# Kernel optimization log

Measured on AMD Instinct MI355X. Metric: run time of the kernel, lower is better.

The kernel has to match this reference:

```python
import jax, jax.numpy as jnp
import numpy as np

N = 50000
E = 800000
IN_DIM = 256
HID = 256
OUT_DIM = 2


def setup_inputs() -> dict:
    key = jax.random.key(0)
    ks = jax.random.split(key, 10)
    x = jax.random.normal(ks[0], (N, IN_DIM), dtype=jnp.float32)
    edge_index = jax.random.randint(ks[1], (2, E), 0, N, dtype=jnp.int64)
    # Glorot-ish scaling so activations stay well-conditioned through 4 layers
    def w(k, fan_in, fan_out):
        return jax.random.normal(k, (fan_in, fan_out), dtype=jnp.float32) / jnp.sqrt(jnp.float32(fan_in))
    return {
        "x": x,
        "edge_index": edge_index,
        "W0": w(ks[2], IN_DIM, HID), "b0": jnp.zeros((HID,), jnp.float32),
        "W1": w(ks[3], HID, HID),    "b1": jnp.zeros((HID,), jnp.float32),
        "W2": w(ks[4], HID, HID),    "b2": jnp.zeros((HID,), jnp.float32),
        "W3": w(ks[5], HID, OUT_DIM), "b3": jnp.zeros((OUT_DIM,), jnp.float32),
    }


def _gcn_norm(edge_index, n, dtype):
    # PyG gcn_norm with self-loops: deg over destination, norm = d^-1/2[src]*d^-1/2[dst]
    loops = jnp.arange(n, dtype=edge_index.dtype)
    src = jnp.concatenate([edge_index[0], loops])
    dst = jnp.concatenate([edge_index[1], loops])
    deg = jax.ops.segment_sum(jnp.ones_like(dst, dtype=dtype), dst, num_segments=n)
    dis = deg ** -0.5  # deg >= 1 due to self-loops
    norm = dis[src] * dis[dst]
    return src, dst, norm


def reference(x, edge_index, W0, b0, W1, b1, W2, b2, W3, b3):
    n = x.shape[0]
    src, dst, norm = _gcn_norm(edge_index, n, x.dtype)

    def conv(h, W, b):
        h = h @ W                              # [N, F_out] dense GEMM
        msg = h[src] * norm[:, None]           # edge-gather + scale
        agg = jax.ops.segment_sum(msg, dst, num_segments=n)  # scatter-add
        return agg + b

    h = jax.nn.relu(conv(x, W0, b0))
    h = jax.nn.relu(conv(h, W1, b1))
    h = jax.nn.relu(conv(h, W2, b2))
    return conv(h, W3, b3)
```

## Files before the change

kernel.cpp:

```cpp
#include <hip/hip_runtime.h>

#define N_NODES 50000
#define N_EDGES 800000

static inline int cdiv(int a, int b) { return (a + b - 1) / b; }

typedef __attribute__((ext_vector_type(8))) short bf16x8;
typedef __attribute__((ext_vector_type(4))) float f32x4;
typedef __attribute__((ext_vector_type(2))) float f32x2;
typedef __attribute__((ext_vector_type(4))) unsigned int u32x4;

static __device__ __forceinline__ unsigned short f2bf(float f) {
    unsigned int u = __float_as_uint(f);
    unsigned int r = (u + 0x7FFF + ((u >> 16) & 1)) >> 16;
    return (unsigned short)r;
}
static __device__ __forceinline__ float bf2f(unsigned short h) {
    return __uint_as_float((unsigned int)h << 16);
}
static __device__ __forceinline__ float bf_lo(unsigned int u) { return __uint_as_float(u << 16); }
static __device__ __forceinline__ float bf_hi(unsigned int u) { return __uint_as_float(u & 0xFFFF0000u); }

static __device__ __forceinline__ int2 ldnt2(const int2* p) {
    unsigned long long u = __builtin_nontemporal_load((const unsigned long long*)p);
    int2 r;
    r.x = (int)(u & 0xFFFFFFFFull);
    r.y = (int)(u >> 32);
    return r;
}

static __device__ __forceinline__ void acc8p(f32x2* acc, uint4 v, float wgt) {
    f32x2 w2;
    w2.x = wgt;
    w2.y = wgt;
    f32x2 p;
    p.x = bf_lo(v.x); p.y = bf_hi(v.x); acc[0] += p * w2;
    p.x = bf_lo(v.y); p.y = bf_hi(v.y); acc[1] += p * w2;
    p.x = bf_lo(v.z); p.y = bf_hi(v.z); acc[2] += p * w2;
    p.x = bf_lo(v.w); p.y = bf_hi(v.w); acc[3] += p * w2;
}


__global__ void k_count(const int* __restrict__ edst, int* cnt, int e) {
    int i = (blockIdx.x * 256 + threadIdx.x) * 4;
    if (i + 3 < e) {
        int4 v = *(const int4*)(edst + i);
        atomicAdd(&cnt[v.x], 1);
        atomicAdd(&cnt[v.y], 1);
        atomicAdd(&cnt[v.z], 1);
        atomicAdd(&cnt[v.w], 1);
    } else {
        for (int k = i; k < e; ++k) atomicAdd(&cnt[edst[k]], 1);
    }
}

__global__ __launch_bounds__(256) void k_scan1(const int* __restrict__ cnt,
                                               int* __restrict__ row_ptr,
                                               float* __restrict__ dis,
                                               int* __restrict__ blk, int n) {
    __shared__ int sums[256];
    int t = threadIdx.x;
    int base = blockIdx.x * 1024 + t * 4;
    int c0 = 0, c1 = 0, c2 = 0, c3 = 0;
    if (base + 3 < n) {
        int4 v = *(const int4*)(cnt + base);
        c0 = v.x + 1; c1 = v.y + 1; c2 = v.z + 1; c3 = v.w + 1;
    } else {
        if (base + 0 < n) c0 = cnt[base + 0] + 1;
        if (base + 1 < n) c1 = cnt[base + 1] + 1;
        if (base + 2 < n) c2 = cnt[base + 2] + 1;
        if (base + 3 < n) c3 = cnt[base + 3] + 1;
    }
    int s = c0 + c1 + c2 + c3;
    sums[t] = s;
    __syncthreads();
    int x = s;
    for (int off = 1; off < 256; off <<= 1) {
        int y = (t >= off) ? sums[t - off] : 0;
        __syncthreads();
        x += y;
        sums[t] = x;
        __syncthreads();
    }
    int excl = x - s;
    if (base + 0 < n) { row_ptr[base + 0] = excl;                dis[base + 0] = rsqrtf((float)c0); }
    if (base + 1 < n) { row_ptr[base + 1] = excl + c0;           dis[base + 1] = rsqrtf((float)c1); }
    if (base + 2 < n) { row_ptr[base + 2] = excl + c0 + c1;      dis[base + 2] = rsqrtf((float)c2); }
    if (base + 3 < n) { row_ptr[base + 3] = excl + c0 + c1 + c2; dis[base + 3] = rsqrtf((float)c3); }
    if (t == 255) blk[blockIdx.x] = x;
}

__global__ __launch_bounds__(256) void k_scan2(int* __restrict__ blk,
                                               int* __restrict__ row_ptr_n, int nb) {
    __shared__ int sums[256];
    int t = threadIdx.x;
    int s = (t < nb) ? blk[t] : 0;
    sums[t] = s;
    __syncthreads();
    int x = s;
    for (int off = 1; off < 256; off <<= 1) {
        int y = (t >= off) ? sums[t - off] : 0;
        __syncthreads();
        x += y;
        sums[t] = x;
        __syncthreads();
    }
    if (t < nb) blk[t] = x - s;
    if (t == 255) row_ptr_n[0] = x;
}

__global__ __launch_bounds__(256) void k_scan3(int* __restrict__ row_ptr,
                                               int* __restrict__ pos,
                                               const int* __restrict__ blk, int n) {
    int base = blockIdx.x * 1024 + threadIdx.x * 4;
    int off = blk[blockIdx.x];
#pragma unroll
    for (int i = 0; i < 4; ++i) {
        int idx = base + i;
        if (idx < n) {
            int v = row_ptr[idx] + off;
            row_ptr[idx] = v;
            pos[idx] = v;
        }
    }
}

__global__ void k_fill(const int* __restrict__ esrc, const int* __restrict__ edst,
                       int* pos, const float* __restrict__ dis,
                       int2* __restrict__ eg, int e, int n) {
    int i = blockIdx.x * 256 + threadIdx.x;
    if (i < e) {
        int s = esrc[i], d = edst[i];
        int p = atomicAdd(&pos[d], 1);
        unsigned long long u = (unsigned long long)(unsigned int)s |
                               ((unsigned long long)(unsigned int)__float_as_int(dis[s] * dis[d]) << 32);
        __builtin_nontemporal_store(u, (unsigned long long*)&eg[p]);
    } else if (i < e + n) {
        int v = i - e;
        int p = atomicAdd(&pos[v], 1);
        float dv = dis[v];
        unsigned long long u = (unsigned long long)(unsigned int)v |
                               ((unsigned long long)(unsigned int)__float_as_int(dv * dv) << 32);
        __builtin_nontemporal_store(u, (unsigned long long*)&eg[p]);
    }
}


__global__ __launch_bounds__(256) void k_prep(const float* __restrict__ W0,
                                              const float* __restrict__ W1,
                                              const float* __restrict__ W2,
                                              const float* __restrict__ b0,
                                              const float* __restrict__ b1,
                                              const float* __restrict__ b2,
                                              const float* __restrict__ W3,
                                              unsigned short* __restrict__ Wth,
                                              unsigned short* __restrict__ Wtl,
                                              float* __restrict__ bpw,
                                              const float* __restrict__ X,
                                              unsigned short* __restrict__ Xh, long total4) {
    if (blockIdx.x < 48) {
        __shared__ float tile[64][65];
        int layer = blockIdx.x / 16;
        int tid = blockIdx.x % 16;
        int ti = tid >> 2, tj = tid & 3;
        const float* W = layer == 0 ? W0 : (layer == 1 ? W1 : W2);
        int r0 = ti * 64, n0 = tj * 64;
        int rr = threadIdx.x >> 4;
        int cc = (threadIdx.x & 15) * 4;
#pragma unroll
        for (int j = 0; j < 4; ++j) {
            float4 v = *(const float4*)(W + (size_t)(r0 + rr + j * 16) * 256 + n0 + cc);
            tile[rr + j * 16][cc + 0] = v.x;
            tile[rr + j * 16][cc + 1] = v.y;
            tile[rr + j * 16][cc + 2] = v.z;
            tile[rr + j * 16][cc + 3] = v.w;
        }
        __syncthreads();
        int pl = threadIdx.x & 63;
        int ng = threadIdx.x >> 6;
        int kl = (layer != 0) ? ((pl & 3) * 16 + (pl >> 2)) : pl;
#pragma unroll
        for (int i = 0; i < 16; ++i) {
            int nl = ng * 16 + i;
            float v = tile[kl][nl];
            unsigned short h = f2bf(v);
            size_t o = (size_t)layer * 65536 + (size_t)(n0 + nl) * 256 + r0 + pl;
            Wth[o] = h;
            Wtl[o] = f2bf(v - bf2f(h));
        }
    } else if (blockIdx.x == 48) {
        int p = threadIdx.x;
        int pl = p & 63;
        int c = (p & ~63) + (pl & 3) * 16 + (pl >> 2);
        bpw[p] = b0[c];
        bpw[256 + p] = b1[c];
        bpw[512 + p] = b2[c];
        bpw[768 + p * 2 + 0] = W3[(size_t)c * 2 + 0];
        bpw[768 + p * 2 + 1] = W3[(size_t)c * 2 + 1];
    } else {
        long i = (long)(blockIdx.x - 49) * 256 + threadIdx.x;
        if (i >= total4) return;
        float4 v = *(const float4*)(X + i * 4);
        ushort4 h;
        h.x = f2bf(v.x);
        h.y = f2bf(v.y);
        h.z = f2bf(v.z);
        h.w = f2bf(v.w);
        *(ushort4*)(Xh + i * 4) = h;
    }
}


#define GEMM_RB 196

__global__ __launch_bounds__(256) void k_gemm_mfma(const unsigned short* __restrict__ Ah,
                                                   const unsigned short* __restrict__ Wth,
                                                   const unsigned short* __restrict__ Wtl,
                                                   unsigned short* __restrict__ C, int M) {
    __shared__ unsigned short Wh[64][264];
    __shared__ unsigned short Wl[64][136];
    int rowblk = blockIdx.x % GEMM_RB;
    int colblk = blockIdx.x / GEMM_RB;
    int c0 = colblk * 64;
    int m0 = rowblk * 256;
    int t = threadIdx.x;
    int sr = t >> 2;

    {
        int hk0 = (t & 3) * 64;
        const unsigned short* gh = Wth + (size_t)(c0 + sr) * 256 + hk0;
        unsigned short* lh = &Wh[sr][hk0];
#pragma unroll
        for (int i = 0; i < 8; ++i)
            *(uint4*)(lh + i * 8) = *(const uint4*)(gh + i * 8);
        int lk0 = (t & 3) * 32;
        const unsigned short* gl = Wtl + (size_t)(c0 + sr) * 256 + lk0;
        unsigned short* ll = &Wl[sr][lk0];
#pragma unroll
        for (int i = 0; i < 4; ++i)
            *(uint4*)(ll + i * 8) = *(const uint4*)(gl + i * 8);
    }
    __syncthreads();

    int lane = t & 63, wave = t >> 6;
    int quad = lane >> 4, l16 = lane & 15;

    const unsigned short* aph[4];
#pragma unroll
    for (int mt = 0; mt < 4; ++mt) {
        int m = m0 + wave * 64 + mt * 16 + l16;
        if (m >= M) m = M - 1;
        aph[mt] = Ah + (size_t)m * 256 + quad * 8;
    }

    f32x4 acc[4][4];
#pragma unroll
    for (int i = 0; i < 4; ++i)
#pragma unroll
        for (int j = 0; j < 4; ++j) acc[i][j] = (f32x4){0.f, 0.f, 0.f, 0.f};

#pragma unroll 2
    for (int kc = 0; kc < 4; ++kc) {
        int ko = kc * 32;
        bf16x8 ahf[4];
#pragma unroll
        for (int mt = 0; mt < 4; ++mt) ahf[mt] = *(const bf16x8*)(aph[mt] + ko);
#pragma unroll
        for (int nt = 0; nt < 4; ++nt) {
            bf16x8 bh = *(const bf16x8*)&Wh[nt * 16 + l16][ko + quad * 8];
            bf16x8 bl = *(const bf16x8*)&Wl[nt * 16 + l16][ko + quad * 8];
#pragma unroll
            for (int mt = 0; mt < 4; ++mt) {
                acc[mt][nt] = __builtin_amdgcn_mfma_f32_16x16x32_bf16(ahf[mt], bh, acc[mt][nt], 0, 0, 0);
                acc[mt][nt] = __builtin_amdgcn_mfma_f32_16x16x32_bf16(ahf[mt], bl, acc[mt][nt], 0, 0, 0);
            }
        }
    }

    __syncthreads();
    {
        int lk0 = (t & 3) * 32;
        const unsigned short* gl = Wtl + (size_t)(c0 + sr) * 256 + 128 + lk0;
        unsigned short* ll = &Wl[sr][lk0];
#pragma unroll
        for (int i = 0; i < 4; ++i)
            *(uint4*)(ll + i * 8) = *(const uint4*)(gl + i * 8);
    }
    __syncthreads();

#pragma unroll 2
    for (int kc = 4; kc < 8; ++kc) {
        int ko = kc * 32;
        int kol = ko - 128;
        bf16x8 ahf[4];
#pragma unroll
        for (int mt = 0; mt < 4; ++mt) ahf[mt] = *(const bf16x8*)(aph[mt] + ko);
#pragma unroll
        for (int nt = 0; nt < 4; ++nt) {
            bf16x8 bh = *(const bf16x8*)&Wh[nt * 16 + l16][ko + quad * 8];
            bf16x8 bl = *(const bf16x8*)&Wl[nt * 16 + l16][kol + quad * 8];
#pragma unroll
            for (int mt = 0; mt < 4; ++mt) {
                acc[mt][nt] = __builtin_amdgcn_mfma_f32_16x16x32_bf16(ahf[mt], bh, acc[mt][nt], 0, 0, 0);
                acc[mt][nt] = __builtin_amdgcn_mfma_f32_16x16x32_bf16(ahf[mt], bl, acc[mt][nt], 0, 0, 0);
            }
        }
    }

#pragma unroll
    for (int mt = 0; mt < 4; ++mt) {
#pragma unroll
        for (int r = 0; r < 4; ++r) {
            int row = m0 + wave * 64 + mt * 16 + quad * 4 + r;
            if (row < M) {
                ushort4 sv;
                sv.x = f2bf(acc[mt][0][r]);
                sv.y = f2bf(acc[mt][1][r]);
                sv.z = f2bf(acc[mt][2][r]);
                sv.w = f2bf(acc[mt][3][r]);
                *(ushort4*)(C + (size_t)row * 256 + c0 + l16 * 4) = sv;
            }
        }
    }
}


template <int MODE>
__global__ __launch_bounds__(256, 8) void k_agg256(const unsigned short* __restrict__ t,
                                                   const int* __restrict__ row_ptr,
                                                   const int2* __restrict__ eg,
                                                   const float* __restrict__ bp,
                                                   unsigned short* __restrict__ outh,
                                                   const float* __restrict__ w3p,
                                                   float* __restrict__ t2, int n) {
    int lane = threadIdx.x & 63;
    int wave = threadIdx.x >> 6;
    int node = blockIdx.x * 4 + wave;
    if (node >= n) return;
    int half = lane >> 5;
    int fl = lane & 31;
    int beg = row_ptr[node], end = row_ptr[node + 1];
    f32x2 acc2[4];
#pragma unroll
    for (int i = 0; i < 4; ++i) { acc2[i].x = 0.f; acc2[i].y = 0.f; }
    const unsigned short* tp = t + fl * 8;

    int e = beg + half;
    for (; e + 10 < end; e += 12) {
        int2 a0 = ldnt2(eg + e), a1 = ldnt2(eg + e + 2), a2 = ldnt2(eg + e + 4);
        int2 a3 = ldnt2(eg + e + 6), a4 = ldnt2(eg + e + 8), a5 = ldnt2(eg + e + 10);
        uint4 v0 = *(const uint4*)(tp + (size_t)a0.x * 256);
        uint4 v1 = *(const uint4*)(tp + (size_t)a1.x * 256);
        uint4 v2 = *(const uint4*)(tp + (size_t)a2.x * 256);
        uint4 v3 = *(const uint4*)(tp + (size_t)a3.x * 256);
        uint4 v4 = *(const uint4*)(tp + (size_t)a4.x * 256);
        uint4 v5 = *(const uint4*)(tp + (size_t)a5.x * 256);
        acc8p(acc2, v0, __int_as_float(a0.y));
        acc8p(acc2, v1, __int_as_float(a1.y));
        acc8p(acc2, v2, __int_as_float(a2.y));
        acc8p(acc2, v3, __int_as_float(a3.y));
        acc8p(acc2, v4, __int_as_float(a4.y));
        acc8p(acc2, v5, __int_as_float(a5.y));
    }
    for (; e + 6 < end; e += 8) {
        int2 a0 = ldnt2(eg + e), a1 = ldnt2(eg + e + 2);
        int2 a2 = ldnt2(eg + e + 4), a3 = ldnt2(eg + e + 6);
        uint4 v0 = *(const uint4*)(tp + (size_t)a0.x * 256);
        uint4 v1 = *(const uint4*)(tp + (size_t)a1.x * 256);
        uint4 v2 = *(const uint4*)(tp + (size_t)a2.x * 256);
        uint4 v3 = *(const uint4*)(tp + (size_t)a3.x * 256);
        acc8p(acc2, v0, __int_as_float(a0.y));
        acc8p(acc2, v1, __int_as_float(a1.y));
        acc8p(acc2, v2, __int_as_float(a2.y));
        acc8p(acc2, v3, __int_as_float(a3.y));
    }
    for (; e + 2 < end; e += 4) {
        int2 a0 = ldnt2(eg + e), a1 = ldnt2(eg + e + 2);
        uint4 v0 = *(const uint4*)(tp + (size_t)a0.x * 256);
        uint4 v1 = *(const uint4*)(tp + (size_t)a1.x * 256);
        acc8p(acc2, v0, __int_as_float(a0.y));
        acc8p(acc2, v1, __int_as_float(a1.y));
    }
    if (e < end) {
        int2 a0 = ldnt2(eg + e);
        uint4 v0 = *(const uint4*)(tp + (size_t)a0.x * 256);
        acc8p(acc2, v0, __int_as_float(a0.y));
    }

    float va[8];
#pragma unroll
    for (int i = 0; i < 4; ++i) { va[2 * i] = acc2[i].x; va[2 * i + 1] = acc2[i].y; }
#pragma unroll
    for (int i = 0; i < 8; ++i) va[i] += __shfl_xor(va[i], 32);

    if (MODE == 0) {
        if (half == 0) {
            float4 bA = *(const float4*)(bp + fl * 8);
            float4 bB = *(const float4*)(bp + fl * 8 + 4);
            float r0 = fmaxf(va[0] + bA.x, 0.f), r1 = fmaxf(va[1] + bA.y, 0.f);
            float r2 = fmaxf(va[2] + bA.z, 0.f), r3 = fmaxf(va[3] + bA.w, 0.f);
            float r4 = fmaxf(va[4] + bB.x, 0.f), r5 = fmaxf(va[5] + bB.y, 0.f);
            float r6 = fmaxf(va[6] + bB.z, 0.f), r7 = fmaxf(va[7] + bB.w, 0.f);
            u32x4 w;
            w.x = (unsigned)f2bf(r0) | ((unsigned)f2bf(r1) << 16);
            w.y = (unsigned)f2bf(r2) | ((unsigned)f2bf(r3) << 16);
            w.z = (unsigned)f2bf(r4) | ((unsigned)f2bf(r5) << 16);
            w.w = (unsigned)f2bf(r6) | ((unsigned)f2bf(r7) << 16);
            __builtin_nontemporal_store(w, (u32x4*)(outh + (size_t)node * 256 + fl * 8));
        }
    } else {
        float4 bA = *(const float4*)(bp + fl * 8);
        float4 bB = *(const float4*)(bp + fl * 8 + 4);
        float r0 = fmaxf(va[0] + bA.x, 0.f), r1 = fmaxf(va[1] + bA.y, 0.f);
        float r2 = fmaxf(va[2] + bA.z, 0.f), r3 = fmaxf(va[3] + bA.w, 0.f);
        float r4 = fmaxf(va[4] + bB.x, 0.f), r5 = fmaxf(va[5] + bB.y, 0.f);
        float r6 = fmaxf(va[6] + bB.z, 0.f), r7 = fmaxf(va[7] + bB.w, 0.f);
        const float* wp = w3p + fl * 16;
        float4 wA = *(const float4*)(wp + 0);
        float4 wB = *(const float4*)(wp + 4);
        float4 wC = *(const float4*)(wp + 8);
        float4 wD = *(const float4*)(wp + 12);
        float s0 = r0 * wA.x + r1 * wA.z + r2 * wB.x + r3 * wB.z +
                   r4 * wC.x + r5 * wC.z + r6 * wD.x + r7 * wD.z;
        float s1 = r0 * wA.y + r1 * wA.w + r2 * wB.y + r3 * wB.w +
                   r4 * wC.y + r5 * wC.w + r6 * wD.y + r7 * wD.w;
#pragma unroll
        for (int off = 16; off > 0; off >>= 1) {
            s0 += __shfl_xor(s0, off);
            s1 += __shfl_xor(s1, off);
        }
        if (lane == 0) {
            f32x2 o;
            o.x = s0;
            o.y = s1;
            __builtin_nontemporal_store(o, (f32x2*)(t2 + (size_t)node * 2));
        }
    }
}


__global__ void k_agg2(const float* __restrict__ t2,
                       const int* __restrict__ row_ptr,
                       const int2* __restrict__ eg,
                       const float* __restrict__ b3,
                       float* __restrict__ out, int n) {
    int tid = blockIdx.x * 256 + threadIdx.x;
    int node = tid >> 2;
    int sub = tid & 3;
    if (node >= n) return;
    int beg = row_ptr[node], end = row_ptr[node + 1];
    float a0 = 0.f, a1 = 0.f;
    for (int e = beg + sub; e < end; e += 4) {
        int2 m = ldnt2(eg + e);
        float w = __int_as_float(m.y);
        float2 v = *(const float2*)(t2 + (size_t)m.x * 2);
        a0 += w * v.x;
        a1 += w * v.y;
    }
    a0 += __shfl_xor(a0, 1); a1 += __shfl_xor(a1, 1);
    a0 += __shfl_xor(a0, 2); a1 += __shfl_xor(a1, 2);
    if (sub == 0) {
        out[(size_t)node * 2 + 0] = a0 + b3[0];
        out[(size_t)node * 2 + 1] = a1 + b3[1];
    }
}


extern "C" void kernel_launch(void* const* d_in, const int* in_sizes, int n_in,
                              void* d_out, int out_size, void* d_ws, size_t ws_size,
                              hipStream_t stream) {
    const int N = N_NODES, E = N_EDGES;
    const float* x  = (const float*)d_in[0];
    const int* ei   = (const int*)d_in[1];
    const int* esrc = ei;
    const int* edst = ei + E;
    const float* W0 = (const float*)d_in[2];
    const float* b0 = (const float*)d_in[3];
    const float* W1 = (const float*)d_in[4];
    const float* b1 = (const float*)d_in[5];
    const float* W2 = (const float*)d_in[6];
    const float* b2 = (const float*)d_in[7];
    const float* W3 = (const float*)d_in[8];
    const float* b3 = (const float*)d_in[9];
    float* out = (float*)d_out;

    unsigned short* Ahh = (unsigned short*)d_ws;
    unsigned short* Tb  = Ahh + (size_t)N * 256;
    unsigned short* Wth = Tb + (size_t)N * 256;
    unsigned short* Wtl = Wth + 3 * 65536;
    int2*  eg     = (int2*)(Wtl + 3 * 65536);
    float* t2     = (float*)(eg + (E + N));
    float* bpw    = t2 + (size_t)N * 2;
    float* dis    = bpw + 1280;
    int*   cnt    = (int*)(dis + N);
    int*   row_ptr= cnt + N;
    int*   pos    = row_ptr + (N + 1);
    int*   blk    = pos + N;

    const int NB = cdiv(N, 1024);

    hipMemsetAsync(cnt, 0, (size_t)N * sizeof(int), stream);
    k_count<<<cdiv(E, 1024), 256, 0, stream>>>(edst, cnt, E);
    k_scan1<<<NB, 256, 0, stream>>>(cnt, row_ptr, dis, blk, N);
    k_scan2<<<1, 256, 0, stream>>>(blk, row_ptr + N, NB);
    k_scan3<<<NB, 256, 0, stream>>>(row_ptr, pos, blk, N);
    k_fill<<<cdiv(E + N, 256), 256, 0, stream>>>(esrc, edst, pos, dis, eg, E, N);

    const int ggrid = GEMM_RB * 4;
    const int agrid = cdiv(N, 4);
    const long total4 = (long)N * 64;
    const int CA = cdiv((int)total4, 256);

    k_prep<<<49 + CA, 256, 0, stream>>>(W0, W1, W2, b0, b1, b2, W3, Wth, Wtl, bpw, x, Ahh, total4);

    k_gemm_mfma<<<ggrid, 256, 0, stream>>>(Ahh, Wth, Wtl, Tb, N);
    k_agg256<0><<<agrid, 256, 0, stream>>>(Tb, row_ptr, eg, bpw, Ahh, nullptr, nullptr, N);
    k_gemm_mfma<<<ggrid, 256, 0, stream>>>(Ahh, Wth + 65536, Wtl + 65536, Tb, N);
    k_agg256<0><<<agrid, 256, 0, stream>>>(Tb, row_ptr, eg, bpw + 256, Ahh, nullptr, nullptr, N);
    k_gemm_mfma<<<ggrid, 256, 0, stream>>>(Ahh, Wth + 2 * 65536, Wtl + 2 * 65536, Tb, N);
    k_agg256<1><<<agrid, 256, 0, stream>>>(Tb, row_ptr, eg, bpw + 512, nullptr, bpw + 768, t2, N);
    k_agg2<<<cdiv(4 * N, 256), 256, 0, stream>>>(t2, row_ptr, eg, b3, out, N);
}
```

Measured before the change: 466.3 us.

## Fuse degree count into prep kernel and remap GEMM blocks for XCD locality

Merges the edge-degree counting kernel with the weight/input bf16 prep kernel into a single launch, removing one kernel launch and letting the two independent workloads overlap. It also remaps GEMM block indices so the four column blocks sharing a row block run on the same XCD (blockIdx & 7), improving L2 reuse of the A rows. The GEMM grid is rounded up to a multiple of 8 row blocks, which adds a few blocks that exit early.

```diff
diff --git a/kernel.cpp b/kernel.cpp
--- a/kernel.cpp
+++ b/kernel.cpp
@@ -41,18 +41,85 @@
 }
 
 
-__global__ void k_count(const int* __restrict__ edst, int* cnt, int e) {
-    int i = (blockIdx.x * 256 + threadIdx.x) * 4;
-    if (i + 3 < e) {
-        int4 v = *(const int4*)(edst + i);
-        atomicAdd(&cnt[v.x], 1);
-        atomicAdd(&cnt[v.y], 1);
-        atomicAdd(&cnt[v.z], 1);
-        atomicAdd(&cnt[v.w], 1);
+#define CNT_B (((N_EDGES) + 1023) / 1024)
+
+__global__ __launch_bounds__(256) void k_init(const int* __restrict__ edst, int* cnt, int e,
+                                              const float* __restrict__ W0,
+                                              const float* __restrict__ W1,
+                                              const float* __restrict__ W2,
+                                              const float* __restrict__ b0,
+                                              const float* __restrict__ b1,
+                                              const float* __restrict__ b2,
+                                              const float* __restrict__ W3,
+                                              unsigned short* __restrict__ Wth,
+                                              unsigned short* __restrict__ Wtl,
+                                              float* __restrict__ bpw,
+                                              const float* __restrict__ X,
+                                              unsigned short* __restrict__ Xh, long total4) {
+    if (blockIdx.x < CNT_B) {
+        int i = (blockIdx.x * 256 + threadIdx.x) * 4;
+        if (i + 3 < e) {
+            int4 v = *(const int4*)(edst + i);
+            atomicAdd(&cnt[v.x], 1);
+            atomicAdd(&cnt[v.y], 1);
+            atomicAdd(&cnt[v.z], 1);
+            atomicAdd(&cnt[v.w], 1);
+        } else {
+            for (int k = i; k < e; ++k) atomicAdd(&cnt[edst[k]], 1);
+        }
+    } else if (blockIdx.x < CNT_B + 48) {
+        __shared__ float tile[64][65];
+        int wb = blockIdx.x - CNT_B;
+        int layer = wb / 16;
+        int tid = wb % 16;
+        int ti = tid >> 2, tj = tid & 3;
+        const float* W = layer == 0 ? W0 : (layer == 1 ? W1 : W2);
+        int r0 = ti * 64, n0 = tj * 64;
+        int rr = threadIdx.x >> 4;
+        int cc = (threadIdx.x & 15) * 4;
+#pragma unroll
+        for (int j = 0; j < 4; ++j) {
+            float4 v = *(const float4*)(W + (size_t)(r0 + rr + j * 16) * 256 + n0 + cc);
+            tile[rr + j * 16][cc + 0] = v.x;
+            tile[rr + j * 16][cc + 1] = v.y;
+            tile[rr + j * 16][cc + 2] = v.z;
+            tile[rr + j * 16][cc + 3] = v.w;
+        }
+        __syncthreads();
+        int pl = threadIdx.x & 63;
+        int ng = threadIdx.x >> 6;
+        int kl = (layer != 0) ? ((pl & 3) * 16 + (pl >> 2)) : pl;
+#pragma unroll
+        for (int i = 0; i < 16; ++i) {
+            int nl = ng * 16 + i;
+            float v = tile[kl][nl];
+            unsigned short h = f2bf(v);
+            size_t o = (size_t)layer * 65536 + (size_t)(n0 + nl) * 256 + r0 + pl;
+            Wth[o] = h;
+            Wtl[o] = f2bf(v - bf2f(h));
+        }
+    } else if (blockIdx.x == CNT_B + 48) {
+        int p = threadIdx.x;
+        int pl = p & 63;
+        int c = (p & ~63) + (pl & 3) * 16 + (pl >> 2);
+        bpw[p] = b0[c];
+        bpw[256 + p] = b1[c];
+        bpw[512 + p] = b2[c];
+        bpw[768 + p * 2 + 0] = W3[(size_t)c * 2 + 0];
+        bpw[768 + p * 2 + 1] = W3[(size_t)c * 2 + 1];
     } else {
-        for (int k = i; k < e; ++k) atomicAdd(&cnt[edst[k]], 1);
-    }
-}
+        long i = (long)(blockIdx.x - (CNT_B + 49)) * 256 + threadIdx.x;
+        if (i >= total4) return;
+        float4 v = *(const float4*)(X + i * 4);
+        ushort4 h;
+        h.x = f2bf(v.x);
+        h.y = f2bf(v.y);
+        h.z = f2bf(v.z);
+        h.w = f2bf(v.w);
+        *(ushort4*)(Xh + i * 4) = h;
+    }
+}
+
 
 __global__ __launch_bounds__(256) void k_scan1(const int* __restrict__ cnt,
                                                int* __restrict__ row_ptr,
@@ -146,72 +213,8 @@
 }
 
 
-__global__ __launch_bounds__(256) void k_prep(const float* __restrict__ W0,
-                                              const float* __restrict__ W1,
-                                              const float* __restrict__ W2,
-                                              const float* __restrict__ b0,
-                                              const float* __restrict__ b1,
-                                              const float* __restrict__ b2,
-                                              const float* __restrict__ W3,
-                                              unsigned short* __restrict__ Wth,
-                                              unsigned short* __restrict__ Wtl,
-                                              float* __restrict__ bpw,
-                                              const float* __restrict__ X,
-                                              unsigned short* __restrict__ Xh, long total4) {
-    if (blockIdx.x < 48) {
-        __shared__ float tile[64][65];
-        int layer = blockIdx.x / 16;
-        int tid = blockIdx.x % 16;
-        int ti = tid >> 2, tj = tid & 3;
-        const float* W = layer == 0 ? W0 : (layer == 1 ? W1 : W2);
-        int r0 = ti * 64, n0 = tj * 64;
-        int rr = threadIdx.x >> 4;
-        int cc = (threadIdx.x & 15) * 4;
-#pragma unroll
-        for (int j = 0; j < 4; ++j) {
-            float4 v = *(const float4*)(W + (size_t)(r0 + rr + j * 16) * 256 + n0 + cc);
-            tile[rr + j * 16][cc + 0] = v.x;
-            tile[rr + j * 16][cc + 1] = v.y;
-            tile[rr + j * 16][cc + 2] = v.z;
-            tile[rr + j * 16][cc + 3] = v.w;
-        }
-        __syncthreads();
-        int pl = threadIdx.x & 63;
-        int ng = threadIdx.x >> 6;
-        int kl = (layer != 0) ? ((pl & 3) * 16 + (pl >> 2)) : pl;
-#pragma unroll
-        for (int i = 0; i < 16; ++i) {
-            int nl = ng * 16 + i;
-            float v = tile[kl][nl];
-            unsigned short h = f2bf(v);
-            size_t o = (size_t)layer * 65536 + (size_t)(n0 + nl) * 256 + r0 + pl;
-            Wth[o] = h;
-            Wtl[o] = f2bf(v - bf2f(h));
-        }
-    } else if (blockIdx.x == 48) {
-        int p = threadIdx.x;
-        int pl = p & 63;
-        int c = (p & ~63) + (pl & 3) * 16 + (pl >> 2);
-        bpw[p] = b0[c];
-        bpw[256 + p] = b1[c];
-        bpw[512 + p] = b2[c];
-        bpw[768 + p * 2 + 0] = W3[(size_t)c * 2 + 0];
-        bpw[768 + p * 2 + 1] = W3[(size_t)c * 2 + 1];
-    } else {
-        long i = (long)(blockIdx.x - 49) * 256 + threadIdx.x;
-        if (i >= total4) return;
-        float4 v = *(const float4*)(X + i * 4);
-        ushort4 h;
-        h.x = f2bf(v.x);
-        h.y = f2bf(v.y);
-        h.z = f2bf(v.z);
-        h.w = f2bf(v.w);
-        *(ushort4*)(Xh + i * 4) = h;
-    }
-}
-
-
 #define GEMM_RB 196
+#define GEMM_GRID (((GEMM_RB + 7) / 8) * 32)
 
 __global__ __launch_bounds__(256) void k_gemm_mfma(const unsigned short* __restrict__ Ah,
                                                    const unsigned short* __restrict__ Wth,
@@ -219,8 +222,11 @@
                                                    unsigned short* __restrict__ C, int M) {
     __shared__ unsigned short Wh[64][264];
     __shared__ unsigned short Wl[64][136];
-    int rowblk = blockIdx.x % GEMM_RB;
-    int colblk = blockIdx.x / GEMM_RB;
+    int xcd = blockIdx.x & 7;
+    int s5 = blockIdx.x >> 3;
+    int colblk = s5 & 3;
+    int rowblk = (s5 >> 2) * 8 + xcd;
+    if (rowblk >= GEMM_RB) return;
     int c0 = colblk * 64;
     int m0 = rowblk * 256;
     int t = threadIdx.x;
@@ -498,26 +504,25 @@
     int*   blk    = pos + N;
 
     const int NB = cdiv(N, 1024);
+    const long total4 = (long)N * 64;
+    const int CA = cdiv((int)total4, 256);
 
     hipMemsetAsync(cnt, 0, (size_t)N * sizeof(int), stream);
-    k_count<<<cdiv(E, 1024), 256, 0, stream>>>(edst, cnt, E);
+    k_init<<<CNT_B + 49 + CA, 256, 0, stream>>>(edst, cnt, E,
+                                                W0, W1, W2, b0, b1, b2, W3,
+                                                Wth, Wtl, bpw, x, Ahh, total4);
     k_scan1<<<NB, 256, 0, stream>>>(cnt, row_ptr, dis, blk, N);
     k_scan2<<<1, 256, 0, stream>>>(blk, row_ptr + N, NB);
     k_scan3<<<NB, 256, 0, stream>>>(row_ptr, pos, blk, N);
     k_fill<<<cdiv(E + N, 256), 256, 0, stream>>>(esrc, edst, pos, dis, eg, E, N);
 
-    const int ggrid = GEMM_RB * 4;
     const int agrid = cdiv(N, 4);
-    const long total4 = (long)N * 64;
-    const int CA = cdiv((int)total4, 256);
-
-    k_prep<<<49 + CA, 256, 0, stream>>>(W0, W1, W2, b0, b1, b2, W3, Wth, Wtl, bpw, x, Ahh, total4);
-
-    k_gemm_mfma<<<ggrid, 256, 0, stream>>>(Ahh, Wth, Wtl, Tb, N);
+
+    k_gemm_mfma<<<GEMM_GRID, 256, 0, stream>>>(Ahh, Wth, Wtl, Tb, N);
     k_agg256<0><<<agrid, 256, 0, stream>>>(Tb, row_ptr, eg, bpw, Ahh, nullptr, nullptr, N);
-    k_gemm_mfma<<<ggrid, 256, 0, stream>>>(Ahh, Wth + 65536, Wtl + 65536, Tb, N);
+    k_gemm_mfma<<<GEMM_GRID, 256, 0, stream>>>(Ahh, Wth + 65536, Wtl + 65536, Tb, N);
     k_agg256<0><<<agrid, 256, 0, stream>>>(Tb, row_ptr, eg, bpw + 256, Ahh, nullptr, nullptr, N);
-    k_gemm_mfma<<<ggrid, 256, 0, stream>>>(Ahh, Wth + 2 * 65536, Wtl + 2 * 65536, Tb, N);
+    k_gemm_mfma<<<GEMM_GRID, 256, 0, stream>>>(Ahh, Wth + 2 * 65536, Wtl + 2 * 65536, Tb, N);
     k_agg256<1><<<agrid, 256, 0, stream>>>(Tb, row_ptr, eg, bpw + 512, nullptr, bpw + 768, t2, N);
     k_agg2<<<cdiv(4 * N, 256), 256, 0, stream>>>(t2, row_ptr, eg, b3, out, N);
 }
```

Result: no change. 460.8 us, median of 2 (-1.2%).
